# Kernel optimization log

Hardware: AMD Instinct MI355X
Metric: run time of the kernel (lower is better)

## Reference

```python
import jax, jax.numpy as jnp
import numpy as np

B, S, D, V = 2, 2048, 1024, 32000
EPSILON = 5.0


def setup_inputs() -> dict:
    key = jax.random.key(0)
    k1, k2, k3, k4 = jax.random.split(key, 4)
    inputs_embeds = jax.random.normal(k1, (B, S, D), dtype=jnp.float32)
    table = jax.random.normal(k2, (V, D), dtype=jnp.float32)
    # dx-privacy noise: unit-norm Gaussian direction * Gamma(alpha=D, rate=eps*D) scalar sample
    noise_v = jax.random.normal(k3, (B, S, D), dtype=jnp.float32)
    norm = jnp.linalg.norm(noise_v, axis=-1, keepdims=True)
    norm = jnp.where(norm > 0, norm, jnp.ones_like(norm))
    gamma_scale = jax.random.gamma(k4, jnp.float32(D)) / jnp.float32(EPSILON * D)
    noise = gamma_scale * (noise_v / norm)
    return {"inputs_embeds": inputs_embeds, "table": table, "noise": noise}


def reference(inputs_embeds, table, noise):
    # perturb embeddings with precomputed dx-privacy noise (no_grad in original)
    perturbed = inputs_embeds + noise                      # [B,S,D]
    # full similarity matrix vs vocabulary, then nearest-embedding snap
    sims = jnp.einsum('bsd,vd->bsv', perturbed, table)     # [B,S,V]
    max_token = jnp.argmax(sims, axis=-1)                  # [B,S] int
    res = jnp.take(table, max_token, axis=0)               # [B,S,D]
    return res
```

## Files before the change

kernel.cpp:

```cpp
#include <hip/hip_runtime.h>
#include <stdint.h>

#define ROWS 4096
#define DIM 1024
#define VOCAB 32000
#define BM 128
#define BN 128
#define NTILES (VOCAB / BN)
#define NCHUNKS 16
#define SCALE 2048.0f

typedef float floatx4 __attribute__((ext_vector_type(4)));
typedef _Float16 f16x8 __attribute__((ext_vector_type(8)));
typedef _Float16 f16x4 __attribute__((ext_vector_type(4)));

__device__ __forceinline__ void load_lds16(const _Float16* g, _Float16* l) {
    __builtin_amdgcn_global_load_lds(
        (const __attribute__((address_space(1))) uint32_t*)g,
        (__attribute__((address_space(3))) uint32_t*)l, 16, 0, 0);
}

__global__ void init_keys(unsigned long long* __restrict__ keys) {
    int i = blockIdx.x * 256 + threadIdx.x;
    if (i < ROWS) keys[i] = 0ull;
}

__global__ void prep(const float* __restrict__ emb, const float* __restrict__ noi,
                     const float* __restrict__ table,
                     _Float16* __restrict__ Ah, _Float16* __restrict__ Al,
                     _Float16* __restrict__ Bh, _Float16* __restrict__ Bl,
                     unsigned long long* __restrict__ keys) {
    const int bid = blockIdx.x;
    const int ABLK = ROWS * DIM / 8 / 256;
    if (bid < ABLK) {
        if (bid < ROWS / 256) keys[bid * 256 + threadIdx.x] = 0ull;
        size_t i = ((size_t)bid * 256 + threadIdx.x) * 8;
        floatx4 a = *(const floatx4*)(emb + i);
        floatx4 b = *(const floatx4*)(emb + i + 4);
        floatx4 c = *(const floatx4*)(noi + i);
        floatx4 d = *(const floatx4*)(noi + i + 4);
        f16x8 h, l;
#pragma unroll
        for (int j = 0; j < 4; j++) {
            float p = (a[j] + c[j]) * SCALE;
            _Float16 hh = (_Float16)p;
            h[j] = hh; l[j] = (_Float16)(p - (float)hh);
            float q = (b[j] + d[j]) * SCALE;
            _Float16 hq = (_Float16)q;
            h[4 + j] = hq; l[4 + j] = (_Float16)(q - (float)hq);
        }
        *(f16x8*)(Ah + i) = h;
        *(f16x8*)(Al + i) = l;
    } else {
        size_t i = ((size_t)(bid - ABLK) * 256 + threadIdx.x) * 8;
        floatx4 a = *(const floatx4*)(table + i);
        floatx4 b = *(const floatx4*)(table + i + 4);
        f16x8 h, l;
#pragma unroll
        for (int j = 0; j < 4; j++) {
            float p = a[j] * SCALE;
            _Float16 hh = (_Float16)p;
            h[j] = hh; l[j] = (_Float16)(p - (float)hh);
            float q = b[j] * SCALE;
            _Float16 hq = (_Float16)q;
            h[4 + j] = hq; l[4 + j] = (_Float16)(q - (float)hq);
        }
        *(f16x8*)(Bh + i) = h;
        *(f16x8*)(Bl + i) = l;
    }
}

__global__ __launch_bounds__(256, 2) void gemm_argmax_pre(
    const _Float16* __restrict__ Ah, const _Float16* __restrict__ Al,
    const _Float16* __restrict__ Bh, const _Float16* __restrict__ Bl,
    unsigned long long* __restrict__ keys) {
    __shared__ __align__(16) _Float16 sAh[2][BM * 32];
    __shared__ __align__(16) _Float16 sAl[2][BM * 32];
    __shared__ __align__(16) _Float16 sBh[2][BN * 32];
    __shared__ __align__(16) _Float16 sBl[2][BN * 32];
    __shared__ unsigned long long redk[BM];

    const int tid = threadIdx.x;
    const int w = tid >> 6, lane = tid & 63;
    const int quad = lane >> 4, lq = lane & 15;
    const int rb = blockIdx.x / NCHUNKS, chunk = blockIdx.x % NCHUNKS;
    const int row0 = rb * BM;
    const int wmb = (w & 1) * 4, wnb = (w >> 1) * 4;
    const int wm = wmb * 16, wn = wnb * 16;
    const int tstart = chunk * NTILES / NCHUNKS;
    const int tend = (chunk + 1) * NTILES / NCHUNKS;

    if (tid < BM) redk[tid] = 0ull;

    union PF { f16x8 v; _Float16 s[8]; } fidx, fone;
#pragma unroll
    for (int j = 0; j < 8; j++) { fidx.s[j] = (_Float16)0.0f; fone.s[j] = (_Float16)0.0f; }
    if (quad == 0) { fidx.s[0] = (_Float16)(float)lq; fone.s[0] = (_Float16)1.0f; }
    floatx4 c1 = {0.f, 0.f, 0.f, 0.f}, c2 = {0.f, 0.f, 0.f, 0.f};
    c1 = __builtin_amdgcn_mfma_f32_16x16x32_f16(fidx.v, fone.v, c1, 0, 0, 0);
    c2 = __builtin_amdgcn_mfma_f32_16x16x32_f16(fone.v, fidx.v, c2, 0, 0, 0);
    int m_of[4], n_of[4];
#pragma unroll
    for (int r = 0; r < 4; r++) {
        m_of[r] = (int)(c1[r] + 0.5f);
        n_of[r] = (int)(c2[r] + 0.5f);
    }

    const _Float16* gbase = (w == 0) ? (Ah + (size_t)row0 * DIM)
                        : (w == 1) ? (Al + (size_t)row0 * DIM)
                        : (w == 2) ? Bh : Bl;
    _Float16* lbase = (w == 0) ? sAh[0] : (w == 1) ? sAl[0] : (w == 2) ? sBh[0] : sBl[0];
    const size_t g_lane = (size_t)(lane & 15) * DIM + (size_t)(lane >> 4) * 8;
    const int loff = quad * 128 + lq * 8;
    const bool isB = (w >= 2);

    float rmax[16];
    int ridx[16];
#pragma unroll
    for (int i = 0; i < 16; i++) { rmax[i] = -3.4e38f; ridx[i] = 0; }

#define STAGE(buf, t, kt)                                                        \
    do {                                                                         \
        const _Float16* gs_ = gbase + (isB ? (size_t)(t) * BN * DIM : 0)         \
                              + (kt) * 32 + g_lane;                              \
        _Float16* ld_ = lbase + (buf) * (BM * 32);                               \
        _Pragma("unroll")                                                        \
        for (int c_ = 0; c_ < 8; c_++)                                           \
            load_lds16(gs_ + (size_t)(c_ * 16) * DIM, ld_ + c_ * 512);           \
    } while (0)

    int cur = 0;
    STAGE(0, tstart, 0);

    for (int t = tstart; t < tend; ++t) {
        const int n0 = t * BN;
        floatx4 acc[4][4];
#pragma unroll
        for (int mi = 0; mi < 4; mi++)
#pragma unroll
            for (int ni = 0; ni < 4; ni++)
#pragma unroll
                for (int r = 0; r < 4; r++) acc[mi][ni][r] = 0.0f;

        for (int kt = 0; kt < DIM / 32; ++kt) {
            int nt_ = t, nk = kt + 1;
            if (nk == DIM / 32) { nk = 0; ++nt_; }
            if (nt_ < tend) {
                STAGE(cur ^ 1, nt_, nk);
                asm volatile("s_waitcnt vmcnt(8)" ::: "memory");
            } else {
                asm volatile("s_waitcnt vmcnt(0)" ::: "memory");
            }
            __builtin_amdgcn_s_barrier();

            __builtin_amdgcn_s_setprio(1);
            f16x8 ahf[4], alf[4];
#pragma unroll
            for (int i = 0; i < 4; i++) {
                ahf[i] = *(const f16x8*)(&sAh[cur][(wmb + i) * 512 + loff]);
                alf[i] = *(const f16x8*)(&sAl[cur][(wmb + i) * 512 + loff]);
            }
#pragma unroll
            for (int ni = 0; ni < 4; ni++) {
                f16x8 bh = *(const f16x8*)(&sBh[cur][(wnb + ni) * 512 + loff]);
                f16x8 bl = *(const f16x8*)(&sBl[cur][(wnb + ni) * 512 + loff]);
#pragma unroll
                for (int mi = 0; mi < 4; mi++) {
                    acc[mi][ni] = __builtin_amdgcn_mfma_f32_16x16x32_f16(
                        ahf[mi], bh, acc[mi][ni], 0, 0, 0);
                    acc[mi][ni] = __builtin_amdgcn_mfma_f32_16x16x32_f16(
                        ahf[mi], bl, acc[mi][ni], 0, 0, 0);
                    acc[mi][ni] = __builtin_amdgcn_mfma_f32_16x16x32_f16(
                        alf[mi], bh, acc[mi][ni], 0, 0, 0);
                }
            }
            __builtin_amdgcn_s_setprio(0);

            asm volatile("s_waitcnt lgkmcnt(0)" ::: "memory");
            __builtin_amdgcn_s_barrier();
            cur ^= 1;
        }
#pragma unroll
        for (int mi = 0; mi < 4; mi++)
#pragma unroll
            for (int ni = 0; ni < 4; ni++)
#pragma unroll
                for (int r = 0; r < 4; r++) {
                    float v = acc[mi][ni][r];
                    int col = n0 + wn + ni * 16 + n_of[r];
                    int s = mi * 4 + r;
                    if (v > rmax[s] || (v == rmax[s] && col < ridx[s])) {
                        rmax[s] = v;
                        ridx[s] = col;
                    }
                }
    }
#undef STAGE

#pragma unroll
    for (int s = 0; s < 16; ++s) {
        int mi = s >> 2, r = s & 3;
        int rowl = wm + mi * 16 + m_of[r];
        union { float f; uint32_t i; } u;
        u.f = rmax[s];
        uint32_t ord = (u.i & 0x80000000u) ? ~u.i : (u.i | 0x80000000u);
        unsigned long long key =
            ((unsigned long long)ord << 32) | (uint32_t)(~(uint32_t)ridx[s]);
        atomicMax(&redk[rowl], key);
    }
    __syncthreads();
    if (tid < BM) atomicMax(&keys[row0 + tid], redk[tid]);
}

#define BKF 64
#define LDKF 72
#define TILES_PER_WGF 10
#define NCHUNKSF 25

__global__ __launch_bounds__(256, 2) void gemm_argmax_fused(
    const float* __restrict__ emb, const float* __restrict__ noi,
    const float* __restrict__ table, unsigned long long* __restrict__ keys) {
    __shared__ __align__(16) _Float16 Ah[BM * LDKF];
    __shared__ __align__(16) _Float16 Al[BM * LDKF];
    __shared__ __align__(16) _Float16 Bh[BN * LDKF];
    __shared__ __align__(16) _Float16 Bl[BN * LDKF];
    __shared__ unsigned long long redk[BM];

    const int tid = threadIdx.x;
    const int wave = tid >> 6, lane = tid & 63;
    const int quad = lane >> 4, lq = lane & 15;
    const int rb = blockIdx.x / NCHUNKSF, chunk = blockIdx.x % NCHUNKSF;
    const int row0 = rb * BM;
    const int wm = (wave & 1) * 64, wn = (wave >> 1) * 64;

    if (tid < BM) redk[tid] = 0ull;

    union PF { f16x8 v; _Float16 s[8]; } fidx, fone;
#pragma unroll
    for (int j = 0; j < 8; j++) { fidx.s[j] = (_Float16)0.0f; fone.s[j] = (_Float16)0.0f; }
    if (quad == 0) { fidx.s[0] = (_Float16)(float)lq; fone.s[0] = (_Float16)1.0f; }
    floatx4 c1 = {0.f, 0.f, 0.f, 0.f}, c2 = {0.f, 0.f, 0.f, 0.f};
    c1 = __builtin_amdgcn_mfma_f32_16x16x32_f16(fidx.v, fone.v, c1, 0, 0, 0);
    c2 = __builtin_amdgcn_mfma_f32_16x16x32_f16(fone.v, fidx.v, c2, 0, 0, 0);
    int m_of[4], n_of[4];
#pragma unroll
    for (int r = 0; r < 4; r++) {
        m_of[r] = (int)(c1[r] + 0.5f);
        n_of[r] = (int)(c2[r] + 0.5f);
    }

    float rmax[16];
    int ridx[16];
#pragma unroll
    for (int i = 0; i < 16; i++) { rmax[i] = -3.4e38f; ridx[i] = 0; }

    for (int t = 0; t < TILES_PER_WGF; ++t) {
        const int n0 = (chunk * TILES_PER_WGF + t) * BN;
        floatx4 acc[4][4];
#pragma unroll
        for (int mi = 0; mi < 4; mi++)
#pragma unroll
            for (int ni = 0; ni < 4; ni++)
#pragma unroll
                for (int r = 0; r < 4; r++) acc[mi][ni][r] = 0.0f;

        for (int kt = 0; kt < DIM / BKF; ++kt) {
            const int k0 = kt * BKF;
            __syncthreads();
#pragma unroll
            for (int i = 0; i < 8; i++) {
                int c = i * 256 + tid;
                int r = c >> 4, q = c & 15;
                floatx4 e = *(const floatx4*)(emb + (size_t)(row0 + r) * DIM + k0 + q * 4);
                floatx4 n = *(const floatx4*)(noi + (size_t)(row0 + r) * DIM + k0 + q * 4);
                floatx4 b = *(const floatx4*)(table + (size_t)(n0 + r) * DIM + k0 + q * 4);
                f16x4 ah, al, bh, bl;
#pragma unroll
                for (int j = 0; j < 4; j++) {
                    float pa = (e[j] + n[j]) * SCALE;
                    _Float16 h = (_Float16)pa;
                    ah[j] = h;
                    al[j] = (_Float16)(pa - (float)h);
                    float pb = b[j] * SCALE;
                    _Float16 hb = (_Float16)pb;
                    bh[j] = hb;
                    bl[j] = (_Float16)(pb - (float)hb);
                }
                *(f16x4*)(Ah + r * LDKF + q * 4) = ah;
                *(f16x4*)(Al + r * LDKF + q * 4) = al;
                *(f16x4*)(Bh + r * LDKF + q * 4) = bh;
                *(f16x4*)(Bl + r * LDKF + q * 4) = bl;
            }
            __syncthreads();
#pragma unroll
            for (int ks = 0; ks < BKF; ks += 32) {
                f16x8 bhf[4], blf[4], ahf[4], alf[4];
#pragma unroll
                for (int i = 0; i < 4; i++) {
                    bhf[i] = *(const f16x8*)(Bh + (wn + i * 16 + lq) * LDKF + ks + quad * 8);
                    blf[i] = *(const f16x8*)(Bl + (wn + i * 16 + lq) * LDKF + ks + quad * 8);
                    ahf[i] = *(const f16x8*)(Ah + (wm + i * 16 + lq) * LDKF + ks + quad * 8);
                    alf[i] = *(const f16x8*)(Al + (wm + i * 16 + lq) * LDKF + ks + quad * 8);
                }
#pragma unroll
                for (int mi = 0; mi < 4; mi++)
#pragma unroll
                    for (int ni = 0; ni < 4; ni++) {
                        acc[mi][ni] = __builtin_amdgcn_mfma_f32_16x16x32_f16(
                            ahf[mi], bhf[ni], acc[mi][ni], 0, 0, 0);
                        acc[mi][ni] = __builtin_amdgcn_mfma_f32_16x16x32_f16(
                            ahf[mi], blf[ni], acc[mi][ni], 0, 0, 0);
                        acc[mi][ni] = __builtin_amdgcn_mfma_f32_16x16x32_f16(
                            alf[mi], bhf[ni], acc[mi][ni], 0, 0, 0);
                    }
            }
        }
#pragma unroll
        for (int mi = 0; mi < 4; mi++)
#pragma unroll
            for (int ni = 0; ni < 4; ni++)
#pragma unroll
                for (int r = 0; r < 4; r++) {
                    float v = acc[mi][ni][r];
                    int col = n0 + wn + ni * 16 + n_of[r];
                    int s = mi * 4 + r;
                    if (v > rmax[s] || (v == rmax[s] && col < ridx[s])) {
                        rmax[s] = v;
                        ridx[s] = col;
                    }
                }
    }

#pragma unroll
    for (int s = 0; s < 16; ++s) {
        int mi = s >> 2, r = s & 3;
        int rowl = wm + mi * 16 + m_of[r];
        union { float f; uint32_t i; } u;
        u.f = rmax[s];
        uint32_t ord = (u.i & 0x80000000u) ? ~u.i : (u.i | 0x80000000u);
        unsigned long long key =
            ((unsigned long long)ord << 32) | (uint32_t)(~(uint32_t)ridx[s]);
        atomicMax(&redk[rowl], key);
    }
    __syncthreads();
    if (tid < BM) atomicMax(&keys[row0 + tid], redk[tid]);
}

__global__ void gather_kernel(const unsigned long long* __restrict__ keys,
                              const float* __restrict__ table,
                              float* __restrict__ out) {
    int row = blockIdx.x;
    unsigned long long key = keys[row];
    uint32_t ix = ~(uint32_t)(key & 0xFFFFFFFFull);
    const floatx4* src = (const floatx4*)(table + (size_t)ix * DIM);
    floatx4* dst = (floatx4*)(out + (size_t)row * DIM);
    dst[threadIdx.x] = src[threadIdx.x];
}

extern "C" void kernel_launch(void* const* d_in, const int* in_sizes, int n_in,
                              void* d_out, int out_size, void* d_ws, size_t ws_size,
                              hipStream_t stream) {
    (void)in_sizes; (void)n_in; (void)out_size;
    const float* emb = (const float*)d_in[0];
    const float* table = (const float*)d_in[1];
    const float* noi = (const float*)d_in[2];
    float* out = (float*)d_out;

    uint8_t* ws = (uint8_t*)d_ws;
    unsigned long long* keys = (unsigned long long*)ws;
    const size_t keysB = (size_t)ROWS * 8;
    const size_t aB = (size_t)ROWS * DIM * 2;
    const size_t bB = (size_t)VOCAB * DIM * 2;
    const size_t need = keysB + 2 * aB + 2 * bB;

    if (ws_size >= need) {
        _Float16* Ah = (_Float16*)(ws + keysB);
        _Float16* Al = (_Float16*)(ws + keysB + aB);
        _Float16* Bh = (_Float16*)(ws + keysB + 2 * aB);
        _Float16* Bl = (_Float16*)(ws + keysB + 2 * aB + bB);
        const int ablk = ROWS * DIM / 8 / 256;
        const int bblk = VOCAB * DIM / 8 / 256;
        prep<<<ablk + bblk, 256, 0, stream>>>(emb, noi, table, Ah, Al, Bh, Bl, keys);
        gemm_argmax_pre<<<(ROWS / BM) * NCHUNKS, 256, 0, stream>>>(Ah, Al, Bh, Bl, keys);
    } else {
        init_keys<<<ROWS / 256, 256, 0, stream>>>(keys);
        gemm_argmax_fused<<<(ROWS / BM) * NCHUNKSF, 256, 0, stream>>>(emb, noi, table, keys);
    }
    gather_kernel<<<ROWS, 256, 0, stream>>>(keys, table, out);
}
```

Measured before the change: 1.177 ms.

## Drop LDS double buffering and raise occupancy to four blocks per CU

Removes the explicit double-buffered LDS prefetch pipeline and replaces it with a simple load-sync-compute loop over single buffers, halving shared memory per block. The launch bound is raised from 2 to 4 blocks per SM and the vocabulary is split into 32 chunks instead of 16, giving more blocks. The aim is to hide global latency through occupancy instead of software pipelining. In exchange there are two full barriers per k-step with no overlap inside a block, the register budget is tighter, and there are twice as many atomic key merges.

```diff
diff --git a/kernel.cpp b/kernel.cpp
--- a/kernel.cpp
+++ b/kernel.cpp
@@ -7,7 +7,7 @@
 #define BM 128
 #define BN 128
 #define NTILES (VOCAB / BN)
-#define NCHUNKS 16
+#define NCHUNKS 32
 #define SCALE 2048.0f
 
 typedef float floatx4 __attribute__((ext_vector_type(4)));
@@ -70,14 +70,14 @@
     }
 }
 
-__global__ __launch_bounds__(256, 2) void gemm_argmax_pre(
+__global__ __launch_bounds__(256, 4) void gemm_argmax_pre(
     const _Float16* __restrict__ Ah, const _Float16* __restrict__ Al,
     const _Float16* __restrict__ Bh, const _Float16* __restrict__ Bl,
     unsigned long long* __restrict__ keys) {
-    __shared__ __align__(16) _Float16 sAh[2][BM * 32];
-    __shared__ __align__(16) _Float16 sAl[2][BM * 32];
-    __shared__ __align__(16) _Float16 sBh[2][BN * 32];
-    __shared__ __align__(16) _Float16 sBl[2][BN * 32];
+    __shared__ __align__(16) _Float16 sAh[BM * 32];
+    __shared__ __align__(16) _Float16 sAl[BM * 32];
+    __shared__ __align__(16) _Float16 sBh[BN * 32];
+    __shared__ __align__(16) _Float16 sBl[BN * 32];
     __shared__ unsigned long long redk[BM];
 
     const int tid = threadIdx.x;
@@ -109,7 +109,7 @@
     const _Float16* gbase = (w == 0) ? (Ah + (size_t)row0 * DIM)
                         : (w == 1) ? (Al + (size_t)row0 * DIM)
                         : (w == 2) ? Bh : Bl;
-    _Float16* lbase = (w == 0) ? sAh[0] : (w == 1) ? sAl[0] : (w == 2) ? sBh[0] : sBl[0];
+    _Float16* ldst = (w == 0) ? sAh : (w == 1) ? sAl : (w == 2) ? sBh : sBl;
     const size_t g_lane = (size_t)(lane & 15) * DIM + (size_t)(lane >> 4) * 8;
     const int loff = quad * 128 + lq * 8;
     const bool isB = (w >= 2);
@@ -119,21 +119,9 @@
 #pragma unroll
     for (int i = 0; i < 16; i++) { rmax[i] = -3.4e38f; ridx[i] = 0; }
 
-#define STAGE(buf, t, kt)                                                        \
-    do {                                                                         \
-        const _Float16* gs_ = gbase + (isB ? (size_t)(t) * BN * DIM : 0)         \
-                              + (kt) * 32 + g_lane;                              \
-        _Float16* ld_ = lbase + (buf) * (BM * 32);                               \
-        _Pragma("unroll")                                                        \
-        for (int c_ = 0; c_ < 8; c_++)                                           \
-            load_lds16(gs_ + (size_t)(c_ * 16) * DIM, ld_ + c_ * 512);           \
-    } while (0)
-
-    int cur = 0;
-    STAGE(0, tstart, 0);
-
     for (int t = tstart; t < tend; ++t) {
         const int n0 = t * BN;
+        const _Float16* gsrc = gbase + (isB ? (size_t)t * BN * DIM : 0) + g_lane;
         floatx4 acc[4][4];
 #pragma unroll
         for (int mi = 0; mi < 4; mi++)
@@ -143,27 +131,23 @@
                 for (int r = 0; r < 4; r++) acc[mi][ni][r] = 0.0f;
 
         for (int kt = 0; kt < DIM / 32; ++kt) {
-            int nt_ = t, nk = kt + 1;
-            if (nk == DIM / 32) { nk = 0; ++nt_; }
-            if (nt_ < tend) {
-                STAGE(cur ^ 1, nt_, nk);
-                asm volatile("s_waitcnt vmcnt(8)" ::: "memory");
-            } else {
-                asm volatile("s_waitcnt vmcnt(0)" ::: "memory");
+            const int k0 = kt * 32;
+            __syncthreads();
+#pragma unroll
+            for (int c = 0; c < 8; c++)
+                load_lds16(gsrc + (size_t)(c * 16) * DIM + k0, ldst + c * 512);
+            __syncthreads();
+
+            f16x8 ahf[4], alf[4];
+#pragma unroll
+            for (int i = 0; i < 4; i++) {
+                ahf[i] = *(const f16x8*)(&sAh[(wmb + i) * 512 + loff]);
+                alf[i] = *(const f16x8*)(&sAl[(wmb + i) * 512 + loff]);
             }
-            __builtin_amdgcn_s_barrier();
-
-            __builtin_amdgcn_s_setprio(1);
-            f16x8 ahf[4], alf[4];
-#pragma unroll
-            for (int i = 0; i < 4; i++) {
-                ahf[i] = *(const f16x8*)(&sAh[cur][(wmb + i) * 512 + loff]);
-                alf[i] = *(const f16x8*)(&sAl[cur][(wmb + i) * 512 + loff]);
-            }
 #pragma unroll
             for (int ni = 0; ni < 4; ni++) {
-                f16x8 bh = *(const f16x8*)(&sBh[cur][(wnb + ni) * 512 + loff]);
-                f16x8 bl = *(const f16x8*)(&sBl[cur][(wnb + ni) * 512 + loff]);
+                f16x8 bh = *(const f16x8*)(&sBh[(wnb + ni) * 512 + loff]);
+                f16x8 bl = *(const f16x8*)(&sBl[(wnb + ni) * 512 + loff]);
 #pragma unroll
                 for (int mi = 0; mi < 4; mi++) {
                     acc[mi][ni] = __builtin_amdgcn_mfma_f32_16x16x32_f16(
@@ -174,11 +158,6 @@
                         alf[mi], bh, acc[mi][ni], 0, 0, 0);
                 }
             }
-            __builtin_amdgcn_s_setprio(0);
-
-            asm volatile("s_waitcnt lgkmcnt(0)" ::: "memory");
-            __builtin_amdgcn_s_barrier();
-            cur ^= 1;
         }
 #pragma unroll
         for (int mi = 0; mi < 4; mi++)
@@ -195,7 +174,6 @@
                     }
                 }
     }
-#undef STAGE
 
 #pragma unroll
     for (int s = 0; s < 16; ++s) {
```

New measurement: 1.616 ms. 1.37x slower.
